# Kernel tuning notes

Measured on AMD Instinct MI355X. Metric: run time of the kernel, lower is better.

The kernel has to match this reference:

```python
import jax, jax.numpy as jnp
import numpy as np

STOKEN = 16
HEADS = 8


def _unfold(x):
    # torch Unfold(3): identity conv1d, pad 1 -> shifts [x[t-1], x[t], x[t+1]]
    # x: (B, C, M) -> (B, C, 3, M)
    z = jnp.zeros_like(x[:, :, :1])
    xm1 = jnp.concatenate([z, x[:, :, :-1]], axis=-1)
    xp1 = jnp.concatenate([x[:, :, 1:], z], axis=-1)
    return jnp.stack([xm1, x, xp1], axis=2)


def _fold(y):
    # torch Fold(3): identity conv_transpose1d, pad 1 (overlap-add adjoint of _unfold)
    # y: (..., 3, M) -> (..., M); out[s] = y[0, s+1] + y[1, s] + y[2, s-1]
    z0 = jnp.zeros_like(y[..., 0, :1])
    y0 = jnp.concatenate([y[..., 0, 1:], z0], axis=-1)
    y2 = jnp.concatenate([z0, y[..., 2, :-1]], axis=-1)
    return y0 + y[..., 1, :] + y2


def _refine_attention(sf, Wqkv, Wproj, bproj):
    # Attention over super-tokens; sf: (B, C, M)
    B, C, M = sf.shape
    hd = C // HEADS
    qkv = jnp.einsum('oc,bcm->bom', Wqkv, sf).reshape(B, HEADS, 3 * hd, M)
    q, k, v = qkv[:, :, :hd], qkv[:, :, hd:2 * hd], qkv[:, :, 2 * hd:]
    scale = hd ** -0.5
    attn = jnp.einsum('bhdm,bhdn->bhmn', k, q) * scale  # (B,H,M,M), softmax over query axis (faithful)
    attn = jax.nn.softmax(attn, axis=-1)
    out = jnp.einsum('bhdm,bhmn->bhdn', v, attn).reshape(B, C, M)
    return jnp.einsum('oc,bcm->bom', Wproj, out) + bproj[None, :, None]


def setup_inputs() -> dict:
    key = jax.random.key(0)
    k1, k2, k3 = jax.random.split(key, 3)
    B, N, C = 2, 32768, 256
    x = jax.random.normal(k1, (B, N, C), jnp.float32)
    Wqkv = jax.random.normal(k2, (3 * C, C), jnp.float32) * 0.02
    Wproj = jax.random.normal(k3, (C, C), jnp.float32) * 0.02
    bproj = jnp.zeros((C,), jnp.float32)
    return {'x': x, 'Wqkv': Wqkv, 'Wproj': Wproj, 'bproj': bproj}


def reference(x, Wqkv, Wproj, bproj):
    n = STOKEN
    B, N, C = x.shape  # N % n == 0, so no padding branch
    xc = jnp.transpose(x, (0, 2, 1))          # (B, C, N)
    m = N // n
    xw = xc.reshape(B, C, m, n)
    sf = xw.mean(-1)                           # adaptive_avg_pool1d -> (B, C, m)
    pix = jnp.transpose(xw, (0, 2, 3, 1))      # (B, m, n, C)
    scale = C ** -0.5
    # --- n_iter=1 affinity computation (torch.no_grad) ---
    sfu = jnp.transpose(_unfold(sf), (0, 3, 1, 2))             # (B, m, C, 3)
    aff = jax.nn.softmax(jnp.einsum('bmnc,bmck->bmnk', pix, sfu) * scale, axis=-1)
    aff = jax.lax.stop_gradient(aff)                            # (B, m, n, 3)
    aff_sum = _fold(jnp.transpose(aff.sum(2), (0, 2, 1)))       # (B, m)
    aff_sum = jax.lax.stop_gradient(aff_sum)
    # --- super-token features (scatter / overlap-add) ---
    sf2 = jnp.einsum('bmnc,bmnk->bmck', pix, aff)               # (B, m, C, 3)
    sf2 = _fold(jnp.transpose(sf2, (0, 2, 3, 1)))               # (B, C, m)
    sf2 = sf2 / (aff_sum[:, None, :] + 1e-12)
    # --- refine with small attention over super-tokens ---
    sf2 = _refine_attention(sf2, Wqkv, Wproj, bproj)            # (B, C, m)
    # --- broadcast back to pixels (gather) ---
    sfu2 = jnp.transpose(_unfold(sf2), (0, 3, 1, 2))            # (B, m, C, 3)
    pix2 = jnp.einsum('bmck,bmnk->bmcn', sfu2, aff)             # (B, m, C, n)
    out = jnp.transpose(pix2, (0, 2, 1, 3)).reshape(B, C, N)    # (B, C, N)
    return out
```

## Files before the change

kernel.cpp:

```cpp
#include <hip/hip_runtime.h>
#include <hip/hip_bf16.h>

#define BB 2
#define NN 32768
#define CC 256
#define SN 16
#define MM 2048
#define HH 8
#define HD 32
#define PP1 4
#define PPB 4
#define QSCALE 0.17677669529663687f
#define AFFSCALE 0.0625f

typedef unsigned short u16;
typedef __attribute__((ext_vector_type(8))) short bf16x8;
typedef __attribute__((ext_vector_type(4))) float f32x4;
typedef __attribute__((ext_vector_type(4))) unsigned short u16x4;

__device__ __forceinline__ u16 f2bfu(float x) {
    unsigned u = __float_as_uint(x);
    u = (u + 0x7fff + ((u >> 16) & 1)) >> 16;
    return (u16)u;
}

__global__ void k1_sf(const float* __restrict__ x, float* __restrict__ sf) {
    int blk = blockIdx.x;
    int b = blk / MM, j = blk % MM;
    int c = threadIdx.x;
    const float* xp = x + ((size_t)(b*NN + j*SN))*CC + c;
    float s = 0.f;
    #pragma unroll
    for (int i = 0; i < SN; ++i) s += xp[i*CC];
    sf[(size_t)blk*CC + c] = s * (1.0f/16.0f);
}

__global__ void k2_aff(const float* __restrict__ x, const float* __restrict__ sf,
                       float* __restrict__ aff) {
    int blk = blockIdx.x; int b = blk / MM, j = blk % MM;
    __shared__ float sfl[3][CC];
    __shared__ float xl[SN][CC];
    int tid = threadIdx.x;
    #pragma unroll
    for (int k = 0; k < 3; ++k) {
        int w = j + k - 1;
        sfl[k][tid] = (w >= 0 && w < MM) ? sf[((size_t)b*MM + w)*CC + tid] : 0.f;
    }
    for (int idx = tid; idx < SN*64; idx += 256) {
        int i = idx >> 6, c4 = (idx & 63) << 2;
        *(float4*)&xl[i][c4] = *(const float4*)&x[((size_t)(b*NN + j*SN + i))*CC + c4];
    }
    __syncthreads();
    int wave = tid >> 6, lane = tid & 63;
    for (int qi = 0; qi < 4; ++qi) {
        int i = wave*4 + qi;
        float d0=0.f, d1=0.f, d2=0.f;
        #pragma unroll
        for (int cq = 0; cq < 4; ++cq) {
            int c = lane + cq*64;
            float xv = xl[i][c];
            d0 += xv * sfl[0][c];
            d1 += xv * sfl[1][c];
            d2 += xv * sfl[2][c];
        }
        #pragma unroll
        for (int off = 32; off >= 1; off >>= 1) {
            d0 += __shfl_xor(d0, off, 64);
            d1 += __shfl_xor(d1, off, 64);
            d2 += __shfl_xor(d2, off, 64);
        }
        if (lane == 0) {
            float l0 = d0*AFFSCALE, l1 = d1*AFFSCALE, l2 = d2*AFFSCALE;
            float mx = fmaxf(l0, fmaxf(l1, l2));
            float e0 = __expf(l0-mx), e1 = __expf(l1-mx), e2 = __expf(l2-mx);
            float inv = 1.0f/(e0+e1+e2);
            size_t base = ((size_t)blk*SN + i)*3;
            aff[base+0] = e0*inv; aff[base+1] = e1*inv; aff[base+2] = e2*inv;
        }
    }
}

__global__ void k3_sf2(const float* __restrict__ x, const float* __restrict__ aff,
                       float* __restrict__ sf2) {
    int blk = blockIdx.x; int b = blk / MM, j = blk % MM;
    int c = threadIdx.x;
    __shared__ float al[3][SN];
    __shared__ float asum_sh;
    if (threadIdx.x < 48) {
        int k = threadIdx.x / 16, i = threadIdx.x % 16;
        int w = (k == 0) ? j+1 : (k == 1) ? j : j-1;
        al[k][i] = (w >= 0 && w < MM) ? aff[(((size_t)b*MM + w)*SN + i)*3 + k] : 0.f;
    }
    __syncthreads();
    if (threadIdx.x == 0) {
        float s = 0.f;
        for (int t = 0; t < 48; ++t) s += al[t/16][t%16];
        asum_sh = s;
    }
    float acc = 0.f;
    #pragma unroll
    for (int k = 0; k < 3; ++k) {
        int w = (k==0)? j+1 : (k==1)? j : j-1;
        if (w < 0 || w >= MM) continue;
        const float* xp = x + ((size_t)(b*NN + w*SN))*CC + c;
        #pragma unroll
        for (int i = 0; i < SN; ++i) acc += xp[i*CC] * al[k][i];
    }
    __syncthreads();
    sf2[((size_t)b*MM + j)*CC + c] = acc / (asum_sh + 1e-12f);
}

__global__ void k4a_mfma(const float* __restrict__ sf2, const float* __restrict__ wqkv,
                         u16* __restrict__ qh, u16* __restrict__ kh, u16* __restrict__ vth) {
    int mt = blockIdx.x, ot = blockIdx.y, b = blockIdx.z;
    int mm0 = mt*64, oo0 = ot*64;
    __shared__ u16 S[64][264];
    __shared__ u16 W[64][264];
    int tid = threadIdx.x;
    for (int idx = tid; idx < 64*64; idx += 256) {
        int r = idx >> 6, c4 = (idx & 63) << 2;
        float4 sv = *(const float4*)&sf2[((size_t)b*MM + mm0 + r)*CC + c4];
        *(u16x4*)&S[r][c4] = (u16x4){f2bfu(sv.x), f2bfu(sv.y), f2bfu(sv.z), f2bfu(sv.w)};
        float4 wv = *(const float4*)&wqkv[(size_t)(oo0 + r)*CC + c4];
        *(u16x4*)&W[r][c4] = (u16x4){f2bfu(wv.x), f2bfu(wv.y), f2bfu(wv.z), f2bfu(wv.w)};
    }
    __syncthreads();
    int w = tid >> 6, l = tid & 63;
    f32x4 acc[4] = {{0.f,0.f,0.f,0.f},{0.f,0.f,0.f,0.f},{0.f,0.f,0.f,0.f},{0.f,0.f,0.f,0.f}};
    #pragma unroll
    for (int kc = 0; kc < 8; ++kc) {
        bf16x8 bf = *(const bf16x8*)&W[w*16 + (l&15)][kc*32 + ((l>>4)<<3)];
        #pragma unroll
        for (int nt = 0; nt < 4; ++nt) {
            bf16x8 af = *(const bf16x8*)&S[nt*16 + (l&15)][kc*32 + ((l>>4)<<3)];
            acc[nt] = __builtin_amdgcn_mfma_f32_16x16x32_bf16(af, bf, acc[nt], 0, 0, 0);
        }
    }
    int o = oo0 + w*16 + (l&15);
    int h = o / 96, rr = o % 96;
    int bh = b*HH + h;
    int m0 = mm0 + ((l>>4)<<2);
    #pragma unroll
    for (int nt = 0; nt < 4; ++nt) {
        #pragma unroll
        for (int r = 0; r < 4; ++r) {
            int m = m0 + nt*16 + r;
            float v = acc[nt][r];
            if (rr < 32)      qh[((size_t)bh*MM + m)*HD + rr]       = f2bfu(v * QSCALE);
            else if (rr < 64) kh[((size_t)bh*MM + m)*HD + (rr-32)]  = f2bfu(v);
            else              vth[((size_t)bh*HD + (rr-64))*MM + m] = f2bfu(v);
        }
    }
}

__global__ void k4b_mfma(const u16* __restrict__ qh, const u16* __restrict__ kh,
                         float* __restrict__ ses) {
    int bx = blockIdx.x;
    int p = blockIdx.y;
    int bh = bx >> 5;
    int mt = bx & 31;
    int mm0 = mt * 64;
    int tid = threadIdx.x, w = tid >> 6, l = tid & 63;
    bf16x8 af = *(const bf16x8*)&kh[((size_t)bh*MM + mm0 + w*16 + (l&15))*HD + ((l>>4)<<3)];
    __shared__ u16 Qlds[64][40];
    float rs0=0.f, rs1=0.f, rs2=0.f, rs3=0.f;
    int nnbeg = p * (MM/PP1), nnend = nnbeg + (MM/PP1);
    for (int nn0 = nnbeg; nn0 < nnend; nn0 += 64) {
        __syncthreads();
        {
            int r = tid >> 2, ch = tid & 3;
            *(bf16x8*)&Qlds[r][ch*8] =
                *(const bf16x8*)&qh[((size_t)bh*MM + nn0 + r)*HD + ch*8];
        }
        __syncthreads();
        #pragma unroll
        for (int nt = 0; nt < 4; ++nt) {
            bf16x8 bf = *(const bf16x8*)&Qlds[nt*16 + (l&15)][(l>>4)<<3];
            f32x4 acc = {0.f,0.f,0.f,0.f};
            acc = __builtin_amdgcn_mfma_f32_16x16x32_bf16(af, bf, acc, 0, 0, 0);
            rs0 += __expf(acc[0]); rs1 += __expf(acc[1]);
            rs2 += __expf(acc[2]); rs3 += __expf(acc[3]);
        }
    }
    float rs[4] = {rs0, rs1, rs2, rs3};
    #pragma unroll
    for (int r = 0; r < 4; ++r) {
        float v = rs[r];
        v += __shfl_xor(v, 1, 64);
        v += __shfl_xor(v, 2, 64);
        v += __shfl_xor(v, 4, 64);
        v += __shfl_xor(v, 8, 64);
        if ((l & 15) == 0)
            ses[((size_t)p*BB*HH + bh)*MM + mm0 + w*16 + ((l>>4)<<2) + r] = v;
    }
}

__global__ void k4c_mfma(const u16* __restrict__ qh, const u16* __restrict__ kh,
                         const u16* __restrict__ vth, const float* __restrict__ ses,
                         float* __restrict__ part) {
    int bx = blockIdx.x;
    int p = blockIdx.y;
    int bh = bx >> 5;
    int ntile = bx & 31;
    int nn0 = ntile * 64;
    int b = bh >> 3, h = bh & 7;
    int tid = threadIdx.x, w = tid >> 6, l = tid & 63;
    bf16x8 qf[4];
    #pragma unroll
    for (int nt = 0; nt < 4; ++nt)
        qf[nt] = *(const bf16x8*)&qh[((size_t)bh*MM + nn0 + nt*16 + (l&15))*HD + ((l>>4)<<3)];
    __shared__ u16 Klds[64][40];
    __shared__ u16 Vtlds[32][72];
    __shared__ u16 Wlds[64][72];
    __shared__ float Rlds[64];
    f32x4 o0 = {0.f,0.f,0.f,0.f}, o1 = {0.f,0.f,0.f,0.f};
    int mmbeg = p * (MM/PPB), mmend = mmbeg + (MM/PPB);
    const size_t SESP = (size_t)BB*HH*MM;
    for (int mm0 = mmbeg; mm0 < mmend; mm0 += 64) {
        __syncthreads();
        {
            int r = tid >> 2, ch = tid & 3;
            *(bf16x8*)&Klds[r][ch*8] =
                *(const bf16x8*)&kh[((size_t)bh*MM + mm0 + r)*HD + ch*8];
            int d = tid >> 3, ch2 = tid & 7;
            *(bf16x8*)&Vtlds[d][ch2*8] =
                *(const bf16x8*)&vth[((size_t)bh*HD + d)*MM + mm0 + ch2*8];
            if (tid < 64) {
                size_t e = (size_t)bh*MM + mm0 + tid;
                float s = ses[e] + ses[SESP + e] + ses[2*SESP + e] + ses[3*SESP + e];
                Rlds[tid] = 1.0f / s;
            }
        }
        __syncthreads();
        {
            bf16x8 af = *(const bf16x8*)&Klds[w*16 + (l&15)][(l>>4)<<3];
            float ri[4];
            #pragma unroll
            for (int r = 0; r < 4; ++r) ri[r] = Rlds[w*16 + ((l>>4)<<2) + r];
            #pragma unroll
            for (int nt = 0; nt < 4; ++nt) {
                f32x4 s = {0.f,0.f,0.f,0.f};
                s = __builtin_amdgcn_mfma_f32_16x16x32_bf16(af, qf[nt], s, 0, 0, 0);
                unsigned p0 = (unsigned)f2bfu(__expf(s[0]) * ri[0])
                            | ((unsigned)f2bfu(__expf(s[1]) * ri[1]) << 16);
                unsigned p1 = (unsigned)f2bfu(__expf(s[2]) * ri[2])
                            | ((unsigned)f2bfu(__expf(s[3]) * ri[3]) << 16);
                uint2 pk; pk.x = p0; pk.y = p1;
                *(uint2*)&Wlds[nt*16 + (l&15)][w*16 + ((l>>4)<<2)] = pk;
            }
        }
        __syncthreads();
        #pragma unroll
        for (int ks = 0; ks < 2; ++ks) {
            bf16x8 a2 = *(const bf16x8*)&Wlds[w*16 + (l&15)][ks*32 + ((l>>4)<<3)];
            bf16x8 b20 = *(const bf16x8*)&Vtlds[(l&15)][ks*32 + ((l>>4)<<3)];
            bf16x8 b21 = *(const bf16x8*)&Vtlds[16 + (l&15)][ks*32 + ((l>>4)<<3)];
            o0 = __builtin_amdgcn_mfma_f32_16x16x32_bf16(a2, b20, o0, 0, 0, 0);
            o1 = __builtin_amdgcn_mfma_f32_16x16x32_bf16(a2, b21, o1, 0, 0, 0);
        }
    }
    int nnb = nn0 + w*16 + ((l>>4)<<2);
    int dcol = h*32 + (l&15);
    float* op = part + ((size_t)p*BB + b)*((size_t)MM*CC);
    #pragma unroll
    for (int r = 0; r < 4; ++r) {
        op[((size_t)nnb + r)*CC + dcol]      = o0[r];
        op[((size_t)nnb + r)*CC + dcol + 16] = o1[r];
    }
}

__global__ void k5_mfma(const float* __restrict__ part, const float* __restrict__ wproj,
                        const float* __restrict__ bproj, float* __restrict__ sf2r) {
    int mt = blockIdx.x, ot = blockIdx.y, b = blockIdx.z;
    int mm0 = mt*64, oo0 = ot*64;
    __shared__ u16 S[64][264];
    __shared__ u16 W[64][264];
    int tid = threadIdx.x;
    const size_t PARTP = (size_t)BB*MM*CC;
    const float* pb = part + (size_t)b*MM*CC;
    for (int idx = tid; idx < 64*64; idx += 256) {
        int r = idx >> 6, c4 = (idx & 63) << 2;
        size_t e = (size_t)(mm0 + r)*CC + c4;
        float4 s0 = *(const float4*)&pb[e];
        float4 s1 = *(const float4*)&pb[PARTP + e];
        float4 s2 = *(const float4*)&pb[2*PARTP + e];
        float4 s3 = *(const float4*)&pb[3*PARTP + e];
        float sx = s0.x+s1.x+s2.x+s3.x, sy = s0.y+s1.y+s2.y+s3.y;
        float sz = s0.z+s1.z+s2.z+s3.z, sw = s0.w+s1.w+s2.w+s3.w;
        *(u16x4*)&S[r][c4] = (u16x4){f2bfu(sx), f2bfu(sy), f2bfu(sz), f2bfu(sw)};
        float4 wv = *(const float4*)&wproj[(size_t)(oo0 + r)*CC + c4];
        *(u16x4*)&W[r][c4] = (u16x4){f2bfu(wv.x), f2bfu(wv.y), f2bfu(wv.z), f2bfu(wv.w)};
    }
    __syncthreads();
    int w = tid >> 6, l = tid & 63;
    f32x4 acc[4] = {{0.f,0.f,0.f,0.f},{0.f,0.f,0.f,0.f},{0.f,0.f,0.f,0.f},{0.f,0.f,0.f,0.f}};
    #pragma unroll
    for (int kc = 0; kc < 8; ++kc) {
        bf16x8 bf = *(const bf16x8*)&W[w*16 + (l&15)][kc*32 + ((l>>4)<<3)];
        #pragma unroll
        for (int nt = 0; nt < 4; ++nt) {
            bf16x8 af = *(const bf16x8*)&S[nt*16 + (l&15)][kc*32 + ((l>>4)<<3)];
            acc[nt] = __builtin_amdgcn_mfma_f32_16x16x32_bf16(af, bf, acc[nt], 0, 0, 0);
        }
    }
    int o = oo0 + w*16 + (l&15);
    float bp = bproj[o];
    int m0 = mm0 + ((l>>4)<<2);
    #pragma unroll
    for (int nt = 0; nt < 4; ++nt) {
        #pragma unroll
        for (int r = 0; r < 4; ++r) {
            sf2r[((size_t)b*CC + o)*MM + m0 + nt*16 + r] = acc[nt][r] + bp;
        }
    }
}

__global__ void k6_final(const float* __restrict__ sf2r, const float* __restrict__ aff,
                         float* __restrict__ out) {
    int jt = blockIdx.x, cq = blockIdx.y, b = blockIdx.z;
    int jb = jt*16, cq0 = cq*64;
    int tid = threadIdx.x;
    int jl = tid >> 4, il = tid & 15;
    int j = jb + jl;
    size_t abase = (((size_t)b*MM + j)*SN + il)*3;
    float a0 = aff[abase], a1 = aff[abase+1], a2 = aff[abase+2];
    __shared__ float stile[64][18];
    for (int idx = tid; idx < 64*18; idx += 256) {
        int cl = idx / 18, jo = idx % 18;
        int jj = jb - 1 + jo;
        stile[cl][jo] = (jj >= 0 && jj < MM) ? sf2r[((size_t)b*CC + cq0 + cl)*MM + jj] : 0.f;
    }
    __syncthreads();
    int t = jb*SN + tid;
    float* ob = out + (size_t)b*CC*NN + (size_t)cq0*NN + t;
    #pragma unroll 4
    for (int cl = 0; cl < 64; ++cl) {
        float v = stile[cl][jl]*a0 + stile[cl][jl+1]*a1 + stile[cl][jl+2]*a2;
        ob[(size_t)cl*NN] = v;
    }
}

extern "C" void kernel_launch(void* const* d_in, const int* in_sizes, int n_in,
                              void* d_out, int out_size, void* d_ws, size_t ws_size,
                              hipStream_t stream) {
    const float *x = nullptr, *wqkv = nullptr, *wproj = nullptr, *bproj = nullptr;
    for (int i = 0; i < n_in; ++i) {
        int sz = in_sizes[i];
        if (sz == BB*NN*CC)        x     = (const float*)d_in[i];
        else if (sz == 3*CC*CC)    wqkv  = (const float*)d_in[i];
        else if (sz == CC*CC)      wproj = (const float*)d_in[i];
        else if (sz == CC)         bproj = (const float*)d_in[i];
    }
    float* out = (float*)d_out;
    char* ws = (char*)d_ws;
    const size_t MB = 1024*1024;
    float* aff     = (float*)(ws);
    float* regA    = (float*)(ws + 1*MB);
    u16*   qh      = (u16*)  (ws + 5*MB);
    u16*   kh      = (u16*)  (ws + 7*MB);
    u16*   vth     = (u16*)  (ws + 9*MB);
    float* ses     = (float*)(ws + 11*MB);
    float* sf2r    = (float*)(ws + 12*MB);
    float* part    = (float*)(ws + 16*MB);
    float* sf      = regA;
    float* sf2     = regA;

    k1_sf   <<<BB*MM, 256, 0, stream>>>(x, sf);
    k2_aff  <<<BB*MM, 256, 0, stream>>>(x, sf, aff);
    k3_sf2  <<<BB*MM, 256, 0, stream>>>(x, aff, sf2);
    k4a_mfma<<<dim3(MM/64, 12, BB), 256, 0, stream>>>(sf2, wqkv, qh, kh, vth);
    k4b_mfma<<<dim3(BB*HH*(MM/64), PP1), 256, 0, stream>>>(qh, kh, ses);
    k4c_mfma<<<dim3(BB*HH*(MM/64), PPB), 256, 0, stream>>>(qh, kh, vth, ses, part);
    k5_mfma <<<dim3(MM/64, 4, BB), 256, 0, stream>>>(part, wproj, bproj, sf2r);
    k6_final<<<dim3(MM/16, 4, BB), 256, 0, stream>>>(sf2r, aff, out);
}
```

Before: 143.5 us.

## Fuse pooling, affinity and super-token aggregation into one kernel with halo recompute

Merges the three front kernels (window mean, 3-way affinity softmax, and weighted overlap-add) into a single kernel per super-token. Each block loads its own and both neighbour windows of x into shared memory, recomputes the pooled features for five windows and the affinities for three windows, then aggregates locally. This removes two launches and the round trips of sf and aff through global memory. In exchange it does roughly three times the affinity work, reads the outer two windows straight from global memory, and uses about 50KB of shared memory per block, which may reduce occupancy.

After: 182.0 us. +26.8%, slower.

```diff
diff --git a/kernel.cpp b/kernel.cpp
--- a/kernel.cpp
+++ b/kernel.cpp
@@ -24,90 +24,98 @@
     return (u16)u;
 }
 
-__global__ void k1_sf(const float* __restrict__ x, float* __restrict__ sf) {
-    int blk = blockIdx.x;
-    int b = blk / MM, j = blk % MM;
-    int c = threadIdx.x;
-    const float* xp = x + ((size_t)(b*NN + j*SN))*CC + c;
-    float s = 0.f;
-    #pragma unroll
-    for (int i = 0; i < SN; ++i) s += xp[i*CC];
-    sf[(size_t)blk*CC + c] = s * (1.0f/16.0f);
-}
-
-__global__ void k2_aff(const float* __restrict__ x, const float* __restrict__ sf,
-                       float* __restrict__ aff) {
+__global__ void k123(const float* __restrict__ x, float* __restrict__ aff,
+                     float* __restrict__ sf2) {
     int blk = blockIdx.x; int b = blk / MM, j = blk % MM;
-    __shared__ float sfl[3][CC];
-    __shared__ float xl[SN][CC];
+    __shared__ float xl3[3][SN][CC];
+    __shared__ float sf5[5][CC];
+    __shared__ float affl[3][SN][3];
     int tid = threadIdx.x;
-    #pragma unroll
-    for (int k = 0; k < 3; ++k) {
-        int w = j + k - 1;
-        sfl[k][tid] = (w >= 0 && w < MM) ? sf[((size_t)b*MM + w)*CC + tid] : 0.f;
-    }
-    for (int idx = tid; idx < SN*64; idx += 256) {
-        int i = idx >> 6, c4 = (idx & 63) << 2;
-        *(float4*)&xl[i][c4] = *(const float4*)&x[((size_t)(b*NN + j*SN + i))*CC + c4];
+    if (tid < 3*SN*3) ((float*)affl)[tid] = 0.f;
+    for (int idx = tid; idx < 3*SN*64; idx += 256) {
+        int wq = idx / (SN*64); int rem = idx % (SN*64);
+        int i = rem >> 6, c4 = (rem & 63) << 2;
+        int w = j - 1 + wq;
+        float4 v = make_float4(0.f, 0.f, 0.f, 0.f);
+        if (w >= 0 && w < MM)
+            v = *(const float4*)&x[((size_t)(b*NN + w*SN + i))*CC + c4];
+        *(float4*)&xl3[wq][i][c4] = v;
+    }
+    __syncthreads();
+    {
+        int c = tid;
+        #pragma unroll
+        for (int w5 = 0; w5 < 5; ++w5) {
+            float s = 0.f;
+            if (w5 >= 1 && w5 <= 3) {
+                #pragma unroll
+                for (int i = 0; i < SN; ++i) s += xl3[w5-1][i][c];
+            } else {
+                int w = j - 2 + w5;
+                if (w >= 0 && w < MM) {
+                    const float* xp = x + ((size_t)(b*NN + w*SN))*CC + c;
+                    #pragma unroll
+                    for (int i = 0; i < SN; ++i) s += xp[i*CC];
+                }
+            }
+            sf5[w5][c] = s * (1.0f/16.0f);
+        }
     }
     __syncthreads();
     int wave = tid >> 6, lane = tid & 63;
-    for (int qi = 0; qi < 4; ++qi) {
-        int i = wave*4 + qi;
-        float d0=0.f, d1=0.f, d2=0.f;
-        #pragma unroll
-        for (int cq = 0; cq < 4; ++cq) {
-            int c = lane + cq*64;
-            float xv = xl[i][c];
-            d0 += xv * sfl[0][c];
-            d1 += xv * sfl[1][c];
-            d2 += xv * sfl[2][c];
-        }
-        #pragma unroll
-        for (int off = 32; off >= 1; off >>= 1) {
-            d0 += __shfl_xor(d0, off, 64);
-            d1 += __shfl_xor(d1, off, 64);
-            d2 += __shfl_xor(d2, off, 64);
-        }
-        if (lane == 0) {
-            float l0 = d0*AFFSCALE, l1 = d1*AFFSCALE, l2 = d2*AFFSCALE;
-            float mx = fmaxf(l0, fmaxf(l1, l2));
-            float e0 = __expf(l0-mx), e1 = __expf(l1-mx), e2 = __expf(l2-mx);
-            float inv = 1.0f/(e0+e1+e2);
-            size_t base = ((size_t)blk*SN + i)*3;
-            aff[base+0] = e0*inv; aff[base+1] = e1*inv; aff[base+2] = e2*inv;
-        }
-    }
-}
-
-__global__ void k3_sf2(const float* __restrict__ x, const float* __restrict__ aff,
-                       float* __restrict__ sf2) {
-    int blk = blockIdx.x; int b = blk / MM, j = blk % MM;
-    int c = threadIdx.x;
-    __shared__ float al[3][SN];
-    __shared__ float asum_sh;
-    if (threadIdx.x < 48) {
-        int k = threadIdx.x / 16, i = threadIdx.x % 16;
-        int w = (k == 0) ? j+1 : (k == 1) ? j : j-1;
-        al[k][i] = (w >= 0 && w < MM) ? aff[(((size_t)b*MM + w)*SN + i)*3 + k] : 0.f;
-    }
-    __syncthreads();
-    if (threadIdx.x == 0) {
-        float s = 0.f;
-        for (int t = 0; t < 48; ++t) s += al[t/16][t%16];
-        asum_sh = s;
-    }
-    float acc = 0.f;
-    #pragma unroll
-    for (int k = 0; k < 3; ++k) {
-        int w = (k==0)? j+1 : (k==1)? j : j-1;
+    for (int wj = 0; wj < 3; ++wj) {
+        int w = j - 1 + wj;
         if (w < 0 || w >= MM) continue;
-        const float* xp = x + ((size_t)(b*NN + w*SN))*CC + c;
-        #pragma unroll
-        for (int i = 0; i < SN; ++i) acc += xp[i*CC] * al[k][i];
-    }
-    __syncthreads();
-    sf2[((size_t)b*MM + j)*CC + c] = acc / (asum_sh + 1e-12f);
+        for (int qi = 0; qi < 4; ++qi) {
+            int i = wave*4 + qi;
+            float d0=0.f, d1=0.f, d2=0.f;
+            #pragma unroll
+            for (int cq = 0; cq < 4; ++cq) {
+                int c = lane + cq*64;
+                float xv = xl3[wj][i][c];
+                d0 += xv * sf5[wj][c];
+                d1 += xv * sf5[wj+1][c];
+                d2 += xv * sf5[wj+2][c];
+            }
+            #pragma unroll
+            for (int off = 32; off >= 1; off >>= 1) {
+                d0 += __shfl_xor(d0, off, 64);
+                d1 += __shfl_xor(d1, off, 64);
+                d2 += __shfl_xor(d2, off, 64);
+            }
+            if (lane == 0) {
+                float l0 = d0*AFFSCALE, l1 = d1*AFFSCALE, l2 = d2*AFFSCALE;
+                float mx = fmaxf(l0, fmaxf(l1, l2));
+                float e0 = __expf(l0-mx), e1 = __expf(l1-mx), e2 = __expf(l2-mx);
+                float inv = 1.0f/(e0+e1+e2);
+                float a0 = e0*inv, a1 = e1*inv, a2 = e2*inv;
+                affl[wj][i][0] = a0; affl[wj][i][1] = a1; affl[wj][i][2] = a2;
+                if (wj == 1) {
+                    size_t base = (((size_t)b*MM + j)*SN + i)*3;
+                    aff[base+0] = a0; aff[base+1] = a1; aff[base+2] = a2;
+                }
+            }
+        }
+    }
+    __syncthreads();
+    {
+        int c = tid;
+        float asum = 0.f;
+        #pragma unroll
+        for (int k = 0; k < 3; ++k) {
+            #pragma unroll
+            for (int i = 0; i < SN; ++i) asum += affl[2-k][i][k];
+        }
+        float acc = 0.f;
+        #pragma unroll
+        for (int k = 0; k < 3; ++k) {
+            int wj = 2 - k;
+            #pragma unroll
+            for (int i = 0; i < SN; ++i)
+                acc += xl3[wj][i][c] * affl[wj][i][k];
+        }
+        sf2[((size_t)b*MM + j)*CC + c] = acc / (asum + 1e-12f);
+    }
 }
 
 __global__ void k4a_mfma(const float* __restrict__ sf2, const float* __restrict__ wqkv,
@@ -355,19 +363,15 @@
     char* ws = (char*)d_ws;
     const size_t MB = 1024*1024;
     float* aff     = (float*)(ws);
-    float* regA    = (float*)(ws + 1*MB);
+    float* sf2     = (float*)(ws + 1*MB);
     u16*   qh      = (u16*)  (ws + 5*MB);
     u16*   kh      = (u16*)  (ws + 7*MB);
     u16*   vth     = (u16*)  (ws + 9*MB);
     float* ses     = (float*)(ws + 11*MB);
     float* sf2r    = (float*)(ws + 12*MB);
     float* part    = (float*)(ws + 16*MB);
-    float* sf      = regA;
-    float* sf2     = regA;
-
-    k1_sf   <<<BB*MM, 256, 0, stream>>>(x, sf);
-    k2_aff  <<<BB*MM, 256, 0, stream>>>(x, sf, aff);
-    k3_sf2  <<<BB*MM, 256, 0, stream>>>(x, aff, sf2);
+
+    k123    <<<BB*MM, 256, 0, stream>>>(x, aff, sf2);
     k4a_mfma<<<dim3(MM/64, 12, BB), 256, 0, stream>>>(sf2, wqkv, qh, kh, vth);
     k4b_mfma<<<dim3(BB*HH*(MM/64), PP1), 256, 0, stream>>>(qh, kh, ses);
     k4c_mfma<<<dim3(BB*HH*(MM/64), PPB), 256, 0, stream>>>(qh, kh, vth, ses, part);
```

## Fuse super-token scatter into affinity kernel with per-window partials

Applied to the files above, without the earlier changes.

The affinity kernel now also computes, for each window, the three affinity-weighted pixel partial sums and the affinity column sums from the pixels already staged in shared memory. The QKV projection kernel performs the fold (overlap-add of neighbour partials) and the normalisation while loading its input tile. This removes the separate k3 pass, which re-read x three times per window. In exchange a 3*C partial buffer is written and read back, and the workspace regions are reshuffled so that buffers are aliased.

Result: faster. 127.4 us (median of 2 runs) (-11.3%).

```diff
diff --git a/kernel.cpp b/kernel.cpp
--- a/kernel.cpp
+++ b/kernel.cpp
@@ -35,11 +35,13 @@
     sf[(size_t)blk*CC + c] = s * (1.0f/16.0f);
 }
 
-__global__ void k2_aff(const float* __restrict__ x, const float* __restrict__ sf,
-                       float* __restrict__ aff) {
+__global__ void k2p_aff(const float* __restrict__ x, const float* __restrict__ sf,
+                        float* __restrict__ aff, float* __restrict__ P,
+                        float* __restrict__ A) {
     int blk = blockIdx.x; int b = blk / MM, j = blk % MM;
     __shared__ float sfl[3][CC];
     __shared__ float xl[SN][CC];
+    __shared__ float affl[SN][3];
     int tid = threadIdx.x;
     #pragma unroll
     for (int k = 0; k < 3; ++k) {
@@ -74,53 +76,60 @@
             float mx = fmaxf(l0, fmaxf(l1, l2));
             float e0 = __expf(l0-mx), e1 = __expf(l1-mx), e2 = __expf(l2-mx);
             float inv = 1.0f/(e0+e1+e2);
+            float a0 = e0*inv, a1 = e1*inv, a2 = e2*inv;
             size_t base = ((size_t)blk*SN + i)*3;
-            aff[base+0] = e0*inv; aff[base+1] = e1*inv; aff[base+2] = e2*inv;
-        }
-    }
-}
-
-__global__ void k3_sf2(const float* __restrict__ x, const float* __restrict__ aff,
-                       float* __restrict__ sf2) {
-    int blk = blockIdx.x; int b = blk / MM, j = blk % MM;
-    int c = threadIdx.x;
-    __shared__ float al[3][SN];
-    __shared__ float asum_sh;
-    if (threadIdx.x < 48) {
-        int k = threadIdx.x / 16, i = threadIdx.x % 16;
-        int w = (k == 0) ? j+1 : (k == 1) ? j : j-1;
-        al[k][i] = (w >= 0 && w < MM) ? aff[(((size_t)b*MM + w)*SN + i)*3 + k] : 0.f;
-    }
-    __syncthreads();
-    if (threadIdx.x == 0) {
-        float s = 0.f;
-        for (int t = 0; t < 48; ++t) s += al[t/16][t%16];
-        asum_sh = s;
-    }
-    float acc = 0.f;
-    #pragma unroll
-    for (int k = 0; k < 3; ++k) {
-        int w = (k==0)? j+1 : (k==1)? j : j-1;
-        if (w < 0 || w >= MM) continue;
-        const float* xp = x + ((size_t)(b*NN + w*SN))*CC + c;
-        #pragma unroll
-        for (int i = 0; i < SN; ++i) acc += xp[i*CC] * al[k][i];
-    }
-    __syncthreads();
-    sf2[((size_t)b*MM + j)*CC + c] = acc / (asum_sh + 1e-12f);
-}
-
-__global__ void k4a_mfma(const float* __restrict__ sf2, const float* __restrict__ wqkv,
+            aff[base+0] = a0; aff[base+1] = a1; aff[base+2] = a2;
+            affl[i][0] = a0; affl[i][1] = a1; affl[i][2] = a2;
+        }
+    }
+    __syncthreads();
+    {
+        int c = tid;
+        #pragma unroll
+        for (int k = 0; k < 3; ++k) {
+            float p = 0.f;
+            #pragma unroll
+            for (int i = 0; i < SN; ++i) p += xl[i][c] * affl[i][k];
+            P[((size_t)blk*3 + k)*CC + c] = p;
+        }
+        if (tid < 3) {
+            float a = 0.f;
+            #pragma unroll
+            for (int i = 0; i < SN; ++i) a += affl[i][tid];
+            A[(size_t)blk*3 + tid] = a;
+        }
+    }
+}
+
+__global__ void k4a_mfma(const float* __restrict__ P, const float* __restrict__ A,
+                         const float* __restrict__ wqkv,
                          u16* __restrict__ qh, u16* __restrict__ kh, u16* __restrict__ vth) {
     int mt = blockIdx.x, ot = blockIdx.y, b = blockIdx.z;
     int mm0 = mt*64, oo0 = ot*64;
     __shared__ u16 S[64][264];
     __shared__ u16 W[64][264];
+    __shared__ float dn[64];
     int tid = threadIdx.x;
+    if (tid < 64) {
+        int m = mm0 + tid;
+        float a0 = (m+1 < MM) ? A[((size_t)(b*MM + m+1))*3 + 0] : 0.f;
+        float a1 =               A[((size_t)(b*MM + m  ))*3 + 1];
+        float a2 = (m-1 >= 0)  ? A[((size_t)(b*MM + m-1))*3 + 2] : 0.f;
+        dn[tid] = ((a0 + a1) + a2) + 1e-12f;
+    }
+    __syncthreads();
+    const float* Pb = P + (size_t)b*MM*3*CC;
     for (int idx = tid; idx < 64*64; idx += 256) {
         int r = idx >> 6, c4 = (idx & 63) << 2;
-        float4 sv = *(const float4*)&sf2[((size_t)b*MM + mm0 + r)*CC + c4];
-        *(u16x4*)&S[r][c4] = (u16x4){f2bfu(sv.x), f2bfu(sv.y), f2bfu(sv.z), f2bfu(sv.w)};
+        int m = mm0 + r;
+        float4 p0 = make_float4(0.f,0.f,0.f,0.f), p2 = make_float4(0.f,0.f,0.f,0.f);
+        if (m+1 < MM) p0 = *(const float4*)&Pb[((size_t)(m+1)*3 + 0)*CC + c4];
+        float4 p1 = *(const float4*)&Pb[((size_t)m*3 + 1)*CC + c4];
+        if (m-1 >= 0) p2 = *(const float4*)&Pb[((size_t)(m-1)*3 + 2)*CC + c4];
+        float d = dn[r];
+        float sx = ((p0.x+p1.x)+p2.x)/d, sy = ((p0.y+p1.y)+p2.y)/d;
+        float sz = ((p0.z+p1.z)+p2.z)/d, sw = ((p0.w+p1.w)+p2.w)/d;
+        *(u16x4*)&S[r][c4] = (u16x4){f2bfu(sx), f2bfu(sy), f2bfu(sz), f2bfu(sw)};
         float4 wv = *(const float4*)&wqkv[(size_t)(oo0 + r)*CC + c4];
         *(u16x4*)&W[r][c4] = (u16x4){f2bfu(wv.x), f2bfu(wv.y), f2bfu(wv.z), f2bfu(wv.w)};
     }
@@ -355,20 +364,20 @@
     char* ws = (char*)d_ws;
     const size_t MB = 1024*1024;
     float* aff     = (float*)(ws);
-    float* regA    = (float*)(ws + 1*MB);
+    float* sfbuf   = (float*)(ws + 1*MB);
     u16*   qh      = (u16*)  (ws + 5*MB);
     u16*   kh      = (u16*)  (ws + 7*MB);
     u16*   vth     = (u16*)  (ws + 9*MB);
     float* ses     = (float*)(ws + 11*MB);
-    float* sf2r    = (float*)(ws + 12*MB);
-    float* part    = (float*)(ws + 16*MB);
-    float* sf      = regA;
-    float* sf2     = regA;
+    float* A       = (float*)(ws + 11*MB + 512*1024);
+    float* P       = (float*)(ws + 12*MB);
+    float* part    = (float*)(ws + 12*MB);
+    float* sf      = sfbuf;
+    float* sf2r    = sfbuf;
 
     k1_sf   <<<BB*MM, 256, 0, stream>>>(x, sf);
-    k2_aff  <<<BB*MM, 256, 0, stream>>>(x, sf, aff);
-    k3_sf2  <<<BB*MM, 256, 0, stream>>>(x, aff, sf2);
-    k4a_mfma<<<dim3(MM/64, 12, BB), 256, 0, stream>>>(sf2, wqkv, qh, kh, vth);
+    k2p_aff <<<BB*MM, 256, 0, stream>>>(x, sf, aff, P, A);
+    k4a_mfma<<<dim3(MM/64, 12, BB), 256, 0, stream>>>(P, A, wqkv, qh, kh, vth);
     k4b_mfma<<<dim3(BB*HH*(MM/64), PP1), 256, 0, stream>>>(qh, kh, ses);
     k4c_mfma<<<dim3(BB*HH*(MM/64), PPB), 256, 0, stream>>>(qh, kh, vth, ses, part);
     k5_mfma <<<dim3(MM/64, 4, BB), 256, 0, stream>>>(part, wproj, bproj, sf2r);
```
